# Optimization experiments

Measured on AMD Instinct MI355X. Metric: run time of the kernel, lower is better.

## Reference

```python
import jax, jax.numpy as jnp
import numpy as np

EMBED_DIM = 128
N_HASHES = 16
HASH_BITS = 8


def setup_inputs() -> dict:
    key = jax.random.key(0)
    k1, k2 = jax.random.split(key)
    embeddings = jax.random.normal(k1, (4, 4096, EMBED_DIM), dtype=jnp.float32)
    projections = jax.random.normal(k2, (N_HASHES, EMBED_DIM, HASH_BITS), dtype=jnp.float32) / np.sqrt(EMBED_DIM)
    return {"embeddings": embeddings, "projections": projections, "k": 32}


def reference(embeddings, projections, k):
    # embeddings: [B, S, D], projections: [n_hashes, D, hash_bits]
    B, S, D = embeddings.shape

    # Hash codes (computed by the original module but unused for neighbor search)
    hash_codes = (jnp.einsum('bsd,ndh->bnsh', embeddings, projections) > 0).astype(jnp.int32)
    del hash_codes  # dead code in the original forward as well

    # Pairwise Euclidean distances per batch (torch.cdist p=2)
    sq = jnp.sum(embeddings * embeddings, axis=-1)          # [B, S]
    gram = jnp.einsum('bid,bjd->bij', embeddings, embeddings)  # [B, S, S]
    d2 = sq[:, :, None] + sq[:, None, :] - 2.0 * gram
    eye = jnp.eye(S, dtype=bool)
    # set diagonal to +inf (before sqrt, also keeps gradients clean)
    d2 = jnp.where(eye[None], jnp.inf, jnp.maximum(d2, 0.0))
    dist = jnp.sqrt(d2)  # [B, S, S]

    # k smallest (ascending), matching torch.topk(largest=False)
    neg_vals, idx = jax.lax.top_k(-dist, k)
    distances = -neg_vals            # [B, S, k]
    neighbors = idx.astype(jnp.int32)  # [B, S, k]
    return neighbors, distances
```

## Files before the change

### kernel.cpp

```cpp
#include <hip/hip_runtime.h>
#include <hip/hip_bf16.h>
#include <math.h>
#include <stdint.h>

#define BB 4
#define SS 4096
#define DD 128
#define KK 32
#define QB 16
#define CB2 128
#define NC 64
#define FINF __builtin_inff()

typedef __attribute__((ext_vector_type(8))) short short8v;
typedef __attribute__((ext_vector_type(4))) float f32x4;

__device__ __forceinline__ unsigned short f2bf(float x) {
    __hip_bfloat16 h = __float2bfloat16(x);
    return *reinterpret_cast<unsigned short*>(&h);
}

__device__ __forceinline__ void gload16(const void* gsrc, void* ldsdst) {
    __builtin_amdgcn_global_load_lds(
        (const __attribute__((address_space(1))) unsigned int*)gsrc,
        (__attribute__((address_space(3))) unsigned int*)ldsdst, 16, 0, 0);
}

__global__ __launch_bounds__(256)
void prep_kernel(const float* __restrict__ emb, float* __restrict__ sqg,
                 unsigned short* __restrict__ ebf) {
    const int t    = threadIdx.x;
    const int lane = t & 63;
    const int wid  = t >> 6;
    const int grp  = lane >> 4;
    const int gl   = lane & 15;
    const int row  = blockIdx.x * 16 + wid * 4 + grp;
    const float* rp = emb + (size_t)row * DD;

    const float p0 = rp[  0 + gl], p1 = rp[ 16 + gl], p2 = rp[ 32 + gl], p3 = rp[ 48 + gl];
    const float p4 = rp[ 64 + gl], p5 = rp[ 80 + gl], p6 = rp[ 96 + gl], p7 = rp[112 + gl];
    const float t0 = __fmul_rn(p0, p0), t1 = __fmul_rn(p1, p1);
    const float t2 = __fmul_rn(p2, p2), t3 = __fmul_rn(p3, p3);
    const float t4 = __fmul_rn(p4, p4), t5 = __fmul_rn(p5, p5);
    const float t6 = __fmul_rn(p6, p6), t7 = __fmul_rn(p7, p7);
    const float s = __fadd_rn(__fadd_rn(__fadd_rn(t0, t1), __fadd_rn(t2, t3)),
                              __fadd_rn(__fadd_rn(t4, t5), __fadd_rn(t6, t7)));
    const int gbase = lane & 48;
    const float u = __fadd_rn(s, __shfl(s, gbase + ((lane & 15) + 8)));
    const float w = __fadd_rn(u, __shfl(u, gbase + ((lane & 15) + 4)));
    const float w0 = __shfl(w, gbase + 0), w1 = __shfl(w, gbase + 1);
    const float w2 = __shfl(w, gbase + 2), w3 = __shfl(w, gbase + 3);
    if (gl == 0) sqg[row] = __fadd_rn(__fadd_rn(w0, w2), __fadd_rn(w1, w3));

    const float4 va = *(const float4*)(rp + gl * 8);
    const float4 vb = *(const float4*)(rp + gl * 8 + 4);
    short8v pk;
    pk[0] = (short)f2bf(va.x); pk[1] = (short)f2bf(va.y);
    pk[2] = (short)f2bf(va.z); pk[3] = (short)f2bf(va.w);
    pk[4] = (short)f2bf(vb.x); pk[5] = (short)f2bf(vb.y);
    pk[6] = (short)f2bf(vb.z); pk[7] = (short)f2bf(vb.w);
    const int gsw = gl ^ (row & 7);
    *(short8v*)&ebf[(size_t)row * 128 + gsw * 8] = pk;
}

__global__ __launch_bounds__(1024, 8)
void knn_fast4_kernel(const float* __restrict__ emb, const float* __restrict__ sqg,
                      const unsigned short* __restrict__ ebf, float* __restrict__ out) {
    __shared__ unsigned short qsb[QB][128];
    __shared__ unsigned short csb[CB2][128];
    __shared__ float qsf[QB][128];
    __shared__ float keybuf[QB][CB2];
    __shared__ float sqq_s[QB];

    const int t    = threadIdx.x;
    const int lane = t & 63;
    const int wave = t >> 6;
    const int bx   = blockIdx.x;
    const int b    = bx >> 8;
    const int rb   = bx & 255;
    const int R0   = rb * QB;
    const float* embb = emb + (size_t)b * SS * DD;
    const float* sqb  = sqg + (size_t)b * SS;
    const unsigned short* ebfb = ebf + (size_t)b * SS * 128;

    if (wave < 4)
        gload16((const char*)ebfb + (size_t)R0 * 256 + wave * 1024 + lane * 16,
                (char*)&qsb[0][0] + wave * 1024);
    if (t < QB * 32) {
        const int r = t >> 5, c4 = t & 31;
        *(float4*)&qsf[r][c4 * 4] = *(const float4*)(embb + (size_t)(R0 + r) * DD + c4 * 4);
    }
    if (t < QB) sqq_s[t] = sqb[R0 + t];

    float dl = FINF;
    int   il = 0;
    float tau = FINF;

    const int arow = lane & 15;
    const int bcol = (wave & 7) * 16 + (lane & 15);

    #pragma unroll
    for (int c2 = 0; c2 < 2; ++c2)
        gload16((const char*)ebfb + (wave * 2 + c2) * 1024 + lane * 16,
                (char*)&csb[0][0] + (wave * 2 + c2) * 1024);
    __syncthreads();

    for (int tile = 0; tile < SS / CB2; ++tile) {
        const int j0 = tile * CB2;

        if (wave < 8) {
            f32x4 acc = {0.f, 0.f, 0.f, 0.f};
            #pragma unroll
            for (int ks = 0; ks < 4; ++ks) {
                const int kg = ks * 4 + (lane >> 4);
                short8v a  = *(const short8v*)&qsb[arow][(kg ^ (arow & 7)) << 3];
                short8v bf = *(const short8v*)&csb[bcol][(kg ^ (bcol & 7)) << 3];
                acc = __builtin_amdgcn_mfma_f32_16x16x32_bf16(a, bf, acc, 0, 0, 0);
            }
            const float sqcv = sqb[j0 + bcol];
            const int grow_base = (lane >> 4) * 4;
            #pragma unroll
            for (int q = 0; q < 4; ++q) {
                const int grow = grow_base + q;
                float d2v = sqq_s[grow] + sqcv - 2.0f * acc[q];
                if (R0 + grow == j0 + bcol) d2v = FINF;
                keybuf[grow][bcol] = d2v;
            }
        }
        __syncthreads();

        if (tile + 1 < SS / CB2) {
            const size_t base = (size_t)(j0 + CB2) * 256;
            #pragma unroll
            for (int c2 = 0; c2 < 2; ++c2)
                gload16((const char*)ebfb + base + (wave * 2 + c2) * 1024 + lane * 16,
                        (char*)&csb[0][0] + (wave * 2 + c2) * 1024);
        }

        const int r = wave;
        const float v0 = keybuf[r][lane];
        const float v1 = keybuf[r][64 + lane];

        if (tile == 0) {
            unsigned long long pk =
                ((unsigned long long)__float_as_uint(v0) << 32) | (unsigned)(j0 + lane);
            #pragma unroll
            for (int k = 2; k <= 64; k <<= 1) {
                #pragma unroll
                for (int j = k >> 1; j > 0; j >>= 1) {
                    const unsigned long long other = __shfl_xor(pk, j);
                    const bool up = ((lane & k) == 0);
                    const bool lower = ((lane & j) == 0);
                    const bool keepmin = (lower == up);
                    const bool otherSmaller = other < pk;
                    pk = (keepmin == otherSmaller) ? other : pk;
                }
            }
            dl = __uint_as_float((unsigned)(pk >> 32));
            il = (int)(unsigned)(pk & 0xffffffffu);
            tau = __shfl(dl, NC - 1);
            unsigned long long pend1 = __ballot(v1 < tau);
            while (pend1) {
                const int s = __ffsll(pend1) - 1;
                pend1 &= pend1 - 1;
                const float vs = __shfl(v1, s);
                const int js = j0 + 64 + s;
                const float pd = __shfl_up(dl, 1);
                const int   pi = __shfl_up(il, 1);
                const unsigned long long m = __ballot(dl <= vs);
                const int p = __popcll(m);
                if (lane == p)      { dl = vs; il = js; }
                else if (lane > p)  { dl = pd; il = pi; }
            }
            tau = __shfl(dl, NC - 1);
        } else {
            unsigned long long pend0 = __ballot(v0 < tau);
            unsigned long long pend1 = __ballot(v1 < tau);
            while (pend0) {
                const int s = __ffsll(pend0) - 1;
                pend0 &= pend0 - 1;
                const float vs = __shfl(v0, s);
                const int js = j0 + s;
                const float pd = __shfl_up(dl, 1);
                const int   pi = __shfl_up(il, 1);
                const unsigned long long m = __ballot(dl <= vs);
                const int p = __popcll(m);
                if (lane == p)      { dl = vs; il = js; }
                else if (lane > p)  { dl = pd; il = pi; }
            }
            while (pend1) {
                const int s = __ffsll(pend1) - 1;
                pend1 &= pend1 - 1;
                const float vs = __shfl(v1, s);
                const int js = j0 + 64 + s;
                const float pd = __shfl_up(dl, 1);
                const int   pi = __shfl_up(il, 1);
                const unsigned long long m = __ballot(dl <= vs);
                const int p = __popcll(m);
                if (lane == p)      { dl = vs; il = js; }
                else if (lane > p)  { dl = pd; il = pi; }
            }
            tau = __shfl(dl, NC - 1);
        }
        __syncthreads();
    }

    {
        const int r  = wave;
        const int gi = R0 + r;
        const int ce = il;
        const float* cp = embb + (size_t)ce * DD;
        float g = 0.f;
        #pragma unroll 8
        for (int k4 = 0; k4 < 32; ++k4) {
            const float4 qv = *(const float4*)&qsf[r][k4 * 4];
            const float4 cv = *(const float4*)(cp + k4 * 4);
            g = fmaf(qv.x, cv.x, g);
            g = fmaf(qv.y, cv.y, g);
            g = fmaf(qv.z, cv.z, g);
            g = fmaf(qv.w, cv.w, g);
        }
        const float tsum = __fadd_rn(sqq_s[r], sqb[ce]);
        float d2v = __fsub_rn(tsum, __fmul_rn(2.0f, g));
        d2v = fmaxf(d2v, 0.0f);
        const float ke = (float)sqrt((double)d2v);
        int rank = 0;
        for (int c = 0; c < NC; ++c) {
            const float kc = __shfl(ke, c);
            const int   jc = __shfl(ce, c);
            rank += (kc < ke) || (kc == ke && jc < ce);
        }
        if (rank < KK) {
            const size_t o = ((size_t)b * SS + gi) * KK + rank;
            out[o] = (float)ce;
            out[(size_t)BB * SS * KK + o] = ke;
        }
    }
}

extern "C" void kernel_launch(void* const* d_in, const int* in_sizes, int n_in,
                              void* d_out, int out_size, void* d_ws, size_t ws_size,
                              hipStream_t stream) {
    const float* emb = (const float*)d_in[0];
    float* out = (float*)d_out;
    float* sqg = (float*)d_ws;
    (void)in_sizes; (void)n_in; (void)out_size; (void)ws_size;
    unsigned short* ebf = (unsigned short*)((char*)d_ws + 65536);
    prep_kernel<<<dim3(BB * SS / 16), dim3(256), 0, stream>>>(emb, sqg, ebf);
    knn_fast4_kernel<<<dim3(BB * (SS / QB)), dim3(1024), 0, stream>>>(emb, sqg, ebf, out);
}
```

Measured before the change: 354.3 us.

## Software-pipeline MFMA tile compute with previous tile's top-k merge using double buffers

Candidate tiles shrink to 64 columns and both the bf16 candidate tile and the distance key buffer are double-buffered. This lets waves 12-15 compute the next tile's MFMA distances while every wave merges the previous tile into its running top-k list, with one barrier per tile instead of two. All squared norms for the batch are staged in LDS up front so they are no longer read from global memory inside the loop. The cost is twice as many loop iterations and barriers, fewer waves doing MFMA work, and more LDS use, which may reduce occupancy.

Result: no change. 357.4 us (+0.9%).

```diff
diff --git a/kernel.cpp b/kernel.cpp
--- a/kernel.cpp
+++ b/kernel.cpp
@@ -8,7 +8,8 @@
 #define DD 128
 #define KK 32
 #define QB 16
-#define CB2 128
+#define CT 64
+#define NT (SS / CT)
 #define NC 64
 #define FINF __builtin_inff()
 
@@ -64,12 +65,13 @@
 }
 
 __global__ __launch_bounds__(1024, 8)
-void knn_fast4_kernel(const float* __restrict__ emb, const float* __restrict__ sqg,
+void knn_fast5_kernel(const float* __restrict__ emb, const float* __restrict__ sqg,
                       const unsigned short* __restrict__ ebf, float* __restrict__ out) {
     __shared__ unsigned short qsb[QB][128];
-    __shared__ unsigned short csb[CB2][128];
+    __shared__ unsigned short csb[2][CT][128];
     __shared__ float qsf[QB][128];
-    __shared__ float keybuf[QB][CB2];
+    __shared__ float keybuf[2][QB][CT];
+    __shared__ float sqall[SS];
     __shared__ float sqq_s[QB];
 
     const int t    = threadIdx.x;
@@ -86,123 +88,107 @@
     if (wave < 4)
         gload16((const char*)ebfb + (size_t)R0 * 256 + wave * 1024 + lane * 16,
                 (char*)&qsb[0][0] + wave * 1024);
+    gload16((const char*)ebfb + wave * 1024 + lane * 16,
+            (char*)&csb[0][0][0] + wave * 1024);
     if (t < QB * 32) {
         const int r = t >> 5, c4 = t & 31;
         *(float4*)&qsf[r][c4 * 4] = *(const float4*)(embb + (size_t)(R0 + r) * DD + c4 * 4);
     }
+    *(float4*)&sqall[t * 4] = *(const float4*)(sqb + t * 4);
     if (t < QB) sqq_s[t] = sqb[R0 + t];
+    __syncthreads();
 
     float dl = FINF;
     int   il = 0;
     float tau = FINF;
-
     const int arow = lane & 15;
-    const int bcol = (wave & 7) * 16 + (lane & 15);
-
-    #pragma unroll
-    for (int c2 = 0; c2 < 2; ++c2)
-        gload16((const char*)ebfb + (wave * 2 + c2) * 1024 + lane * 16,
-                (char*)&csb[0][0] + (wave * 2 + c2) * 1024);
-    __syncthreads();
-
-    for (int tile = 0; tile < SS / CB2; ++tile) {
-        const int j0 = tile * CB2;
-
-        if (wave < 8) {
+
+    for (int tile = 0; tile < NT; ++tile) {
+        const int par = tile & 1;
+
+        if (tile + 1 < NT)
+            gload16((const char*)ebfb + (size_t)(tile + 1) * 16384 + wave * 1024 + lane * 16,
+                    (char*)&csb[par ^ 1][0][0] + wave * 1024);
+
+        if (wave >= 12) {
+            const int bcol16 = (wave - 12) * 16 + (lane & 15);
+            const int j0 = tile * CT;
             f32x4 acc = {0.f, 0.f, 0.f, 0.f};
             #pragma unroll
             for (int ks = 0; ks < 4; ++ks) {
                 const int kg = ks * 4 + (lane >> 4);
                 short8v a  = *(const short8v*)&qsb[arow][(kg ^ (arow & 7)) << 3];
-                short8v bf = *(const short8v*)&csb[bcol][(kg ^ (bcol & 7)) << 3];
+                short8v bf = *(const short8v*)&csb[par][bcol16][(kg ^ (bcol16 & 7)) << 3];
                 acc = __builtin_amdgcn_mfma_f32_16x16x32_bf16(a, bf, acc, 0, 0, 0);
             }
-            const float sqcv = sqb[j0 + bcol];
+            const float sqcv = sqall[j0 + bcol16];
             const int grow_base = (lane >> 4) * 4;
             #pragma unroll
             for (int q = 0; q < 4; ++q) {
                 const int grow = grow_base + q;
                 float d2v = sqq_s[grow] + sqcv - 2.0f * acc[q];
-                if (R0 + grow == j0 + bcol) d2v = FINF;
-                keybuf[grow][bcol] = d2v;
+                if (R0 + grow == j0 + bcol16) d2v = FINF;
+                keybuf[par][grow][bcol16] = d2v;
             }
         }
+
+        if (tile >= 1) {
+            const int j0p = (tile - 1) * CT;
+            const float v = keybuf[par ^ 1][wave][lane];
+            if (tile == 1) {
+                unsigned long long pk =
+                    ((unsigned long long)__float_as_uint(v) << 32) | (unsigned)(j0p + lane);
+                #pragma unroll
+                for (int k = 2; k <= 64; k <<= 1) {
+                    #pragma unroll
+                    for (int j = k >> 1; j > 0; j >>= 1) {
+                        const unsigned long long other = __shfl_xor(pk, j);
+                        const bool up = ((lane & k) == 0);
+                        const bool lower = ((lane & j) == 0);
+                        const bool keepmin = (lower == up);
+                        const bool otherSmaller = other < pk;
+                        pk = (keepmin == otherSmaller) ? other : pk;
+                    }
+                }
+                dl = __uint_as_float((unsigned)(pk >> 32));
+                il = (int)(unsigned)(pk & 0xffffffffu);
+                tau = __shfl(dl, NC - 1);
+            } else {
+                unsigned long long pend = __ballot(v < tau);
+                while (pend) {
+                    const int s = __ffsll(pend) - 1;
+                    pend &= pend - 1;
+                    const float vs = __shfl(v, s);
+                    const int js = j0p + s;
+                    const float pd = __shfl_up(dl, 1);
+                    const int   pi = __shfl_up(il, 1);
+                    const unsigned long long m = __ballot(dl <= vs);
+                    const int p = __popcll(m);
+                    if (lane == p)      { dl = vs; il = js; }
+                    else if (lane > p)  { dl = pd; il = pi; }
+                }
+                tau = __shfl(dl, NC - 1);
+            }
+        }
         __syncthreads();
-
-        if (tile + 1 < SS / CB2) {
-            const size_t base = (size_t)(j0 + CB2) * 256;
-            #pragma unroll
-            for (int c2 = 0; c2 < 2; ++c2)
-                gload16((const char*)ebfb + base + (wave * 2 + c2) * 1024 + lane * 16,
-                        (char*)&csb[0][0] + (wave * 2 + c2) * 1024);
-        }
-
-        const int r = wave;
-        const float v0 = keybuf[r][lane];
-        const float v1 = keybuf[r][64 + lane];
-
-        if (tile == 0) {
-            unsigned long long pk =
-                ((unsigned long long)__float_as_uint(v0) << 32) | (unsigned)(j0 + lane);
-            #pragma unroll
-            for (int k = 2; k <= 64; k <<= 1) {
-                #pragma unroll
-                for (int j = k >> 1; j > 0; j >>= 1) {
-                    const unsigned long long other = __shfl_xor(pk, j);
-                    const bool up = ((lane & k) == 0);
-                    const bool lower = ((lane & j) == 0);
-                    const bool keepmin = (lower == up);
-                    const bool otherSmaller = other < pk;
-                    pk = (keepmin == otherSmaller) ? other : pk;
-                }
-            }
-            dl = __uint_as_float((unsigned)(pk >> 32));
-            il = (int)(unsigned)(pk & 0xffffffffu);
-            tau = __shfl(dl, NC - 1);
-            unsigned long long pend1 = __ballot(v1 < tau);
-            while (pend1) {
-                const int s = __ffsll(pend1) - 1;
-                pend1 &= pend1 - 1;
-                const float vs = __shfl(v1, s);
-                const int js = j0 + 64 + s;
-                const float pd = __shfl_up(dl, 1);
-                const int   pi = __shfl_up(il, 1);
-                const unsigned long long m = __ballot(dl <= vs);
-                const int p = __popcll(m);
-                if (lane == p)      { dl = vs; il = js; }
-                else if (lane > p)  { dl = pd; il = pi; }
-            }
-            tau = __shfl(dl, NC - 1);
-        } else {
-            unsigned long long pend0 = __ballot(v0 < tau);
-            unsigned long long pend1 = __ballot(v1 < tau);
-            while (pend0) {
-                const int s = __ffsll(pend0) - 1;
-                pend0 &= pend0 - 1;
-                const float vs = __shfl(v0, s);
-                const int js = j0 + s;
-                const float pd = __shfl_up(dl, 1);
-                const int   pi = __shfl_up(il, 1);
-                const unsigned long long m = __ballot(dl <= vs);
-                const int p = __popcll(m);
-                if (lane == p)      { dl = vs; il = js; }
-                else if (lane > p)  { dl = pd; il = pi; }
-            }
-            while (pend1) {
-                const int s = __ffsll(pend1) - 1;
-                pend1 &= pend1 - 1;
-                const float vs = __shfl(v1, s);
-                const int js = j0 + 64 + s;
-                const float pd = __shfl_up(dl, 1);
-                const int   pi = __shfl_up(il, 1);
-                const unsigned long long m = __ballot(dl <= vs);
-                const int p = __popcll(m);
-                if (lane == p)      { dl = vs; il = js; }
-                else if (lane > p)  { dl = pd; il = pi; }
-            }
-            tau = __shfl(dl, NC - 1);
-        }
-        __syncthreads();
+    }
+
+    {
+        const int j0p = (NT - 1) * CT;
+        const float v = keybuf[(NT - 1) & 1][wave][lane];
+        unsigned long long pend = __ballot(v < tau);
+        while (pend) {
+            const int s = __ffsll(pend) - 1;
+            pend &= pend - 1;
+            const float vs = __shfl(v, s);
+            const int js = j0p + s;
+            const float pd = __shfl_up(dl, 1);
+            const int   pi = __shfl_up(il, 1);
+            const unsigned long long m = __ballot(dl <= vs);
+            const int p = __popcll(m);
+            if (lane == p)      { dl = vs; il = js; }
+            else if (lane > p)  { dl = pd; il = pi; }
+        }
     }
 
     {
@@ -220,7 +206,7 @@
             g = fmaf(qv.z, cv.z, g);
             g = fmaf(qv.w, cv.w, g);
         }
-        const float tsum = __fadd_rn(sqq_s[r], sqb[ce]);
+        const float tsum = __fadd_rn(sqq_s[r], sqall[ce]);
         float d2v = __fsub_rn(tsum, __fmul_rn(2.0f, g));
         d2v = fmaxf(d2v, 0.0f);
         const float ke = (float)sqrt((double)d2v);
@@ -247,5 +233,5 @@
     (void)in_sizes; (void)n_in; (void)out_size; (void)ws_size;
     unsigned short* ebf = (unsigned short*)((char*)d_ws + 65536);
     prep_kernel<<<dim3(BB * SS / 16), dim3(256), 0, stream>>>(emb, sqg, ebf);
-    knn_fast4_kernel<<<dim3(BB * (SS / QB)), dim3(1024), 0, stream>>>(emb, sqg, ebf, out);
-}
+    knn_fast5_kernel<<<dim3(BB * (SS / QB)), dim3(1024), 0, stream>>>(emb, sqg, ebf, out);
+}
```
